# Kernel optimization log

Measured on AMD Instinct MI355X. Metric: run time of the kernel, lower is better.

Reference implementation:

```python
import jax, jax.numpy as jnp
import numpy as np

N = 200000
C = 128
VOX = 0.05
EPS = 1e-5
OFFSETS = np.array([[dz, dy, dx] for dz in (-1, 0, 1) for dy in (-1, 0, 1) for dx in (-1, 0, 1)], dtype=np.int64)


def setup_inputs() -> dict:
    key = jax.random.key(0)
    ks = jax.random.split(key, 8)
    gp = jax.random.normal(ks[0], (N, 14), jnp.float32)
    # ---- voxelization tables (int constants, computed once in numpy) ----
    pts = np.asarray(gp[:, :3], dtype=np.float64)
    vc = np.floor(pts / VOX).astype(np.int64)
    vc = vc - vc.min(axis=0)
    mx = vc.max(axis=0) + 1
    h = vc[:, 0] * mx[1] * mx[2] + vc[:, 1] * mx[2] + vc[:, 2]
    uh, inv = np.unique(h, return_inverse=True)
    M = int(uh.shape[0])
    vcoord = np.zeros((M, 3), np.int64)
    vcoord[inv] = vc  # coords identical for same hash
    nbr_idx = np.zeros((M, 27), np.int32)
    nbr_mask = np.zeros((M, 27), np.float32)
    for o in range(27):
        nc = vcoord + OFFSETS[o]
        inb = (nc >= 0).all(1) & (nc < mx).all(1)
        nh = nc[:, 0] * mx[1] * mx[2] + nc[:, 1] * mx[2] + nc[:, 2]
        pos = np.clip(np.searchsorted(uh, nh), 0, M - 1)
        found = inb & (uh[pos] == nh)
        nbr_idx[:, o] = np.where(found, pos, 0)
        nbr_mask[:, o] = found.astype(np.float32)
    s = 0.05
    return {
        'gaussian_params': gp,
        'w_enc': jax.random.normal(ks[1], (14, C), jnp.float32) * s,
        'b_enc': jnp.zeros((C,), jnp.float32),
        'ln_g': jnp.ones((C,), jnp.float32),
        'ln_b': jnp.zeros((C,), jnp.float32),
        'conv_w': jax.random.normal(ks[2], (4, 27, C, C), jnp.float32) * s,
        'bn_g': jnp.ones((4, C), jnp.float32),
        'bn_b': jnp.zeros((4, C), jnp.float32),
        'w1': jax.random.normal(ks[3], (C, C // 2), jnp.float32) * s,
        'b1': jnp.zeros((C // 2,), jnp.float32),
        'w2': jax.random.normal(ks[4], (C // 2, 14), jnp.float32) * s,
        'b2': jnp.zeros((14,), jnp.float32),
        'nbr_mask': jnp.asarray(nbr_mask),
        'inv_idx': jnp.asarray(inv.astype(np.int32)),
        'nbr_idx': jnp.asarray(nbr_idx),
        'num_voxels': M,
    }


def _bn(x, g, b):
    m = x.mean(0)
    v = x.var(0)
    return (x - m) * jax.lax.rsqrt(v + EPS) * g + b


def _subm(x, W, nbr_idx, nbr_mask):
    # submanifold 3x3x3 conv: sum over 27 offsets of masked neighbor gather @ W[o]
    out = jnp.zeros_like(x)
    for o in range(27):
        out = out + (x[nbr_idx[:, o]] * nbr_mask[:, o:o + 1]) @ W[o]
    return out


def _forward(gp, w_enc, b_enc, ln_g, ln_b, conv_w, bn_g, bn_b, w1, b1, w2, b2, nbr_mask, inv_idx, nbr_idx, num_voxels):
    # input encoder: Linear -> LayerNorm -> ReLU
    f = gp @ w_enc + b_enc
    mu = f.mean(-1, keepdims=True)
    var = f.var(-1, keepdims=True)
    f = jax.nn.relu((f - mu) * jax.lax.rsqrt(var + EPS) * ln_g + ln_b)
    # points -> voxels: segment mean (the op the torch code did with a Python loop)
    cnt = jax.ops.segment_sum(jnp.ones((gp.shape[0],), f.dtype), inv_idx, num_segments=num_voxels)
    x = jax.ops.segment_sum(f, inv_idx, num_segments=num_voxels) / cnt[:, None]
    # 2 residual sparse conv blocks (BN uses batch stats, training-mode forward)
    for blk in range(2):
        idn = x
        out = _subm(x, conv_w[2 * blk], nbr_idx, nbr_mask)
        out = jax.nn.relu(_bn(out, bn_g[2 * blk], bn_b[2 * blk]))
        out = _subm(out, conv_w[2 * blk + 1], nbr_idx, nbr_mask)
        x = jax.nn.relu(_bn(out, bn_g[2 * blk + 1], bn_b[2 * blk + 1]) + idn)
    # voxels -> points, output head, residual add
    pf = x[inv_idx]
    delta = jax.nn.relu(pf @ w1 + b1) @ w2 + b2
    return gp[:, :14] + delta


def reference(gaussian_params, w_enc, b_enc, ln_g, ln_b, conv_w, bn_g, bn_b, w1, b1, w2, b2, nbr_mask, inv_idx, nbr_idx, num_voxels):
    return _forward(gaussian_params, w_enc, b_enc, ln_g, ln_b, conv_w, bn_g, bn_b, w1, b1, w2, b2, nbr_mask, inv_idx, nbr_idx, num_voxels)
```

## Files before the change

### kernel.cpp

```cpp
#include <hip/hip_runtime.h>

typedef __bf16 bf16x8 __attribute__((ext_vector_type(8)));
typedef float f32x16 __attribute__((ext_vector_type(16)));

#define LN_EPS 1e-5f
#define AS1 __attribute__((address_space(1)))
#define AS3 __attribute__((address_space(3)))

__device__ __forceinline__ unsigned f2bf_rne(float f) {
    unsigned x = __float_as_uint(f);
    return (x + 0x7fffu + ((x >> 16) & 1u)) >> 16;
}

__device__ __forceinline__ float bf2f(unsigned short u) {
    return __uint_as_float((unsigned)u << 16);
}

__global__ void pack_w_kernel(const float* __restrict__ cw, unsigned short* __restrict__ Wp, int E) {
    int idx = blockIdx.x * 256 + threadIdx.x;
    if (idx >= E) return;
    float v = cw[idx];
    int n  = idx & 127;
    int c  = (idx >> 7) & 127;
    int oc = idx >> 14;
    Wp[oc * 16384 + (c >> 3) * 1024 + n * 8 + (c & 7)] = (unsigned short)f2bf_rne(v);
}

__global__ void pack_w1_kernel(const float* __restrict__ w1, unsigned short* __restrict__ Wp1) {
    int idx = blockIdx.x * 256 + threadIdx.x;
    if (idx >= 8192) return;
    int k = idx >> 6, n = idx & 63;
    Wp1[(k >> 3) * 512 + n * 8 + (k & 7)] = (unsigned short)f2bf_rne(w1[k * 64 + n]);
}

__global__ void prep_nbr_kernel(const int* __restrict__ nbr_idx, const float* __restrict__ nbr_mask,
                                int* __restrict__ T, unsigned* __restrict__ act, int M) {
    int m = blockIdx.x * 256 + threadIdx.x;
    if (m >= M) return;
    unsigned bits = 0;
#pragma unroll
    for (int o = 0; o < 27; ++o) {
        bool f = nbr_mask[m * 27 + o] != 0.f;
        int g = f ? nbr_idx[m * 27 + o] : M;
        T[o * M + m] = g;
        bits |= (f ? 1u : 0u) << o;
    }
    atomicOr(&act[m >> 8], bits);
}

__global__ __launch_bounds__(256) void encode_kernel(
    const float* __restrict__ gp, const float* __restrict__ w_enc,
    const float* __restrict__ b_enc, const float* __restrict__ ln_g,
    const float* __restrict__ ln_b, const int* __restrict__ inv_idx,
    float* __restrict__ vsum, float* __restrict__ cnt, int N)
{
    int p = blockIdx.x * 4 + (threadIdx.x >> 6);
    int lane = threadIdx.x & 63;
    if (p >= N) return;
    float gv[14];
#pragma unroll
    for (int i = 0; i < 14; ++i) gv[i] = gp[p * 14 + i];
    float f0 = b_enc[lane], f1 = b_enc[lane + 64];
#pragma unroll
    for (int i = 0; i < 14; ++i) {
        f0 = fmaf(gv[i], w_enc[i * 128 + lane], f0);
        f1 = fmaf(gv[i], w_enc[i * 128 + lane + 64], f1);
    }
    float s = f0 + f1;
#pragma unroll
    for (int off = 32; off; off >>= 1) s += __shfl_xor(s, off);
    float mean = s * 0.0078125f;
    float d0 = f0 - mean, d1 = f1 - mean;
    float v = d0 * d0 + d1 * d1;
#pragma unroll
    for (int off = 32; off; off >>= 1) v += __shfl_xor(v, off);
    float rs = rsqrtf(v * 0.0078125f + LN_EPS);
    float h0 = d0 * rs * ln_g[lane] + ln_b[lane];
    float h1 = d1 * rs * ln_g[lane + 64] + ln_b[lane + 64];
    h0 = h0 > 0.f ? h0 : 0.f;
    h1 = h1 > 0.f ? h1 : 0.f;
    int vx = inv_idx[p];
    atomicAdd(&vsum[vx * 128 + lane], h0);
    atomicAdd(&vsum[vx * 128 + lane + 64], h1);
    if (lane == 0) atomicAdd(&cnt[vx], 1.0f);
}

__global__ void vox_mean_kernel(const float* __restrict__ vsum, const float* __restrict__ cnt,
                                unsigned short* __restrict__ out, int total4) {
    int idx = blockIdx.x * 256 + threadIdx.x;
    if (idx >= total4) return;
    int e0 = idx * 4;
    float r = 1.f / cnt[e0 >> 7];
    float4 v = *(const float4*)(vsum + e0);
    uint2 pk;
    pk.x = f2bf_rne(v.x * r) | (f2bf_rne(v.y * r) << 16);
    pk.y = f2bf_rne(v.z * r) | (f2bf_rne(v.w * r) << 16);
    *(uint2*)(out + e0) = pk;
}

#define STAGE_W(OFF, BUFSEL)                                                          \
    {                                                                                 \
        const uint4* WpO4 = (const uint4*)Wp + (OFF) * 2048;                          \
        _Pragma("unroll")                                                             \
        for (int rep = 0; rep < 8; ++rep) {                                           \
            __builtin_amdgcn_global_load_lds(                                         \
                (const AS1 unsigned int*)(WpO4 + rep * 256 + tid),                    \
                (AS3 unsigned int*)(Ws + (BUFSEL) * 2048 + rep * 256 + w * 64),       \
                16, 0, 0);                                                            \
        }                                                                             \
    }

#define GATHER_A(AF, G)                                                               \
    _Pragma("unroll")                                                                 \
    for (int j = 0; j < 8; ++j) (AF)[j] = xin4[(G) * 16 + 2 * j + q];

__global__ __launch_bounds__(256, 2) void subm_conv_kernel(
    const unsigned short* __restrict__ xin,
    const unsigned short* __restrict__ Wp,
    const int* __restrict__ T, const unsigned* __restrict__ act,
    float* __restrict__ yout, float* __restrict__ stats, int M)
{
    __shared__ uint4 Ws[4096];

    const int tid = threadIdx.x;
    const int lane = tid & 63;
    const int w = tid >> 6;

    const int nwg = gridDim.x;
    const int orig = blockIdx.x;
    const int xcd = orig & 7;
    const int q8 = nwg >> 3, r8 = nwg & 7;
    const int tile = (xcd < r8 ? xcd * (q8 + 1) : r8 * (q8 + 1) + (xcd - r8) * q8) + (orig >> 3);

    const int m0 = tile * 256;
    const int rw = w * 64;
    const int q = lane >> 5;
    const int l31 = lane & 31;
    int row0 = m0 + rw + l31;
    int row1 = row0 + 32;
    if (row0 >= M) row0 = M - 1;
    if (row1 >= M) row1 = M - 1;

    f32x16 acc0[4], acc1[4];
#pragma unroll
    for (int t = 0; t < 4; ++t)
#pragma unroll
        for (int r = 0; r < 16; ++r) { acc0[t][r] = 0.f; acc1[t][r] = 0.f; }

    const uint4* xin4 = (const uint4*)xin;
    unsigned amask = act[tile];

    if (amask) {
        int o = __ffs(amask) - 1; amask &= amask - 1;
        STAGE_W(o, 0);
        int g0 = T[o * M + row0];
        int g1 = T[o * M + row1];
        int buf = 0;

        while (true) {
            int onext = -1;
            if (amask) { onext = __ffs(amask) - 1; amask &= amask - 1; }

            __syncthreads();

            if (onext >= 0) STAGE_W(onext, buf ^ 1);

            uint4 af0[8], af1[8];
            GATHER_A(af0, g0);
            GATHER_A(af1, g1);

            int gn0 = 0, gn1 = 0;
            if (onext >= 0) { gn0 = T[onext * M + row0]; gn1 = T[onext * M + row1]; }

            const bf16x8* WsB = (const bf16x8*)(Ws + buf * 2048);
            __builtin_amdgcn_s_setprio(1);
#pragma unroll
            for (int ks = 0; ks < 8; ++ks) {
                int kb = (ks << 1) | q;
                bf16x8 a0 = *(const bf16x8*)&af0[ks];
                bf16x8 a1 = *(const bf16x8*)&af1[ks];
#pragma unroll
                for (int tn = 0; tn < 4; ++tn) {
                    bf16x8 b = WsB[kb * 128 + tn * 32 + l31];
                    acc0[tn] = __builtin_amdgcn_mfma_f32_32x32x16_bf16(a0, b, acc0[tn], 0, 0, 0);
                    acc1[tn] = __builtin_amdgcn_mfma_f32_32x32x16_bf16(a1, b, acc1[tn], 0, 0, 0);
                }
            }
            __builtin_amdgcn_s_setprio(0);

            if (onext < 0) break;
            o = onext; g0 = gn0; g1 = gn1; buf ^= 1;
        }
    }

#pragma unroll
    for (int tn = 0; tn < 4; ++tn) {
        int col = tn * 32 + l31;
        float s = 0.f, sq = 0.f;
#pragma unroll
        for (int r = 0; r < 16; ++r) {
            int rloc = (r & 3) + 8 * (r >> 2) + 4 * q + rw;
            int grow = m0 + rloc;
            float v = (grow < M) ? acc0[tn][r] : 0.f;
            if (grow < M) yout[grow * 128 + col] = v;
            s += v; sq += v * v;
        }
#pragma unroll
        for (int r = 0; r < 16; ++r) {
            int rloc = (r & 3) + 8 * (r >> 2) + 4 * q + rw + 32;
            int grow = m0 + rloc;
            float v = (grow < M) ? acc1[tn][r] : 0.f;
            if (grow < M) yout[grow * 128 + col] = v;
            s += v; sq += v * v;
        }
        s += __shfl_xor(s, 32);
        sq += __shfl_xor(sq, 32);
        if (lane < 32) {
            atomicAdd(&stats[col], s);
            atomicAdd(&stats[128 + col], sq);
        }
    }
}

__global__ void bn_relu_kernel(const float* __restrict__ y, const float* __restrict__ stats,
                               const float* __restrict__ g, const float* __restrict__ b,
                               unsigned short* __restrict__ out, int total4, float invM) {
    int idx = blockIdx.x * 256 + threadIdx.x;
    if (idx >= total4) return;
    int e0 = idx * 4;
    int c0 = e0 & 127;
    float4 yv = *(const float4*)(y + e0);
    float h[4];
    const float* yp = (const float*)&yv;
#pragma unroll
    for (int j = 0; j < 4; ++j) {
        int c = c0 + j;
        float mean = stats[c] * invM;
        float var = stats[128 + c] * invM - mean * mean;
        float sc = g[c] * rsqrtf(var + LN_EPS);
        float sh = b[c] - mean * sc;
        float vv = yp[j] * sc + sh;
        h[j] = vv > 0.f ? vv : 0.f;
    }
    uint2 pk;
    pk.x = f2bf_rne(h[0]) | (f2bf_rne(h[1]) << 16);
    pk.y = f2bf_rne(h[2]) | (f2bf_rne(h[3]) << 16);
    *(uint2*)(out + e0) = pk;
}

__global__ void bn_relu_res_kernel(const float* __restrict__ y, const float* __restrict__ stats,
                                   const float* __restrict__ g, const float* __restrict__ b,
                                   const unsigned short* __restrict__ idn,
                                   unsigned short* __restrict__ out, int total4, float invM) {
    int idx = blockIdx.x * 256 + threadIdx.x;
    if (idx >= total4) return;
    int e0 = idx * 4;
    int c0 = e0 & 127;
    float4 yv = *(const float4*)(y + e0);
    uint2 iv = *(const uint2*)(idn + e0);
    float id[4];
    id[0] = __uint_as_float(iv.x << 16);
    id[1] = __uint_as_float(iv.x & 0xffff0000u);
    id[2] = __uint_as_float(iv.y << 16);
    id[3] = __uint_as_float(iv.y & 0xffff0000u);
    float h[4];
    const float* yp = (const float*)&yv;
#pragma unroll
    for (int j = 0; j < 4; ++j) {
        int c = c0 + j;
        float mean = stats[c] * invM;
        float var = stats[128 + c] * invM - mean * mean;
        float sc = g[c] * rsqrtf(var + LN_EPS);
        float sh = b[c] - mean * sc;
        float vv = yp[j] * sc + sh + id[j];
        h[j] = vv > 0.f ? vv : 0.f;
    }
    uint2 pk;
    pk.x = f2bf_rne(h[0]) | (f2bf_rne(h[1]) << 16);
    pk.y = f2bf_rne(h[2]) | (f2bf_rne(h[3]) << 16);
    *(uint2*)(out + e0) = pk;
}

__global__ __launch_bounds__(256) void head_vox_kernel(
    const unsigned short* __restrict__ A,
    const unsigned short* __restrict__ Wp1,
    const float* __restrict__ b1, const float* __restrict__ w2,
    const float* __restrict__ b2, float* __restrict__ Dv, int M)
{
    __shared__ uint4 W1s[1024];
    __shared__ unsigned short Hs[8192];
    __shared__ float w2s[896];

    const int tid = threadIdx.x;
    const int lane = tid & 63;
    const int w = tid >> 6;
    const int m0 = blockIdx.x * 128;
    const int rw = w * 32;
    const int q = lane >> 5;
    const int l31 = lane & 31;
    int myrow = m0 + rw + l31;
    if (myrow > M) myrow = M;

#pragma unroll
    for (int rep = 0; rep < 4; ++rep) {
        __builtin_amdgcn_global_load_lds(
            (const AS1 unsigned int*)((const uint4*)Wp1 + rep * 256 + tid),
            (AS3 unsigned int*)(W1s + rep * 256 + w * 64), 16, 0, 0);
    }
    for (int i = tid; i < 896; i += 256) w2s[i] = w2[i];

    const uint4* xin4 = (const uint4*)A;
    uint4 af[8];
#pragma unroll
    for (int j = 0; j < 8; ++j) af[j] = xin4[myrow * 16 + 2 * j + q];

    f32x16 acc[2];
#pragma unroll
    for (int t = 0; t < 2; ++t)
#pragma unroll
        for (int r = 0; r < 16; ++r) acc[t][r] = 0.f;

    __syncthreads();

#pragma unroll
    for (int ks = 0; ks < 8; ++ks) {
        int kb = (ks << 1) | q;
        bf16x8 a = *(const bf16x8*)&af[ks];
#pragma unroll
        for (int tn = 0; tn < 2; ++tn) {
            bf16x8 b = ((const bf16x8*)W1s)[kb * 64 + tn * 32 + l31];
            acc[tn] = __builtin_amdgcn_mfma_f32_32x32x16_bf16(a, b, acc[tn], 0, 0, 0);
        }
    }

#pragma unroll
    for (int tn = 0; tn < 2; ++tn) {
        int col = tn * 32 + l31;
        float bias = b1[col];
        int ch = col >> 3, ce = col & 7;
#pragma unroll
        for (int r = 0; r < 16; ++r) {
            int rloc = (r & 3) + 8 * (r >> 2) + 4 * q + rw;
            float v = acc[tn][r] + bias;
            v = v > 0.f ? v : 0.f;
            Hs[rloc * 64 + (ch ^ (rloc & 7)) * 8 + ce] = (unsigned short)f2bf_rne(v);
        }
    }
    __syncthreads();

    int r2 = tid >> 1;
    int c0 = (tid & 1) * 7;
    float o[7];
#pragma unroll
    for (int j = 0; j < 7; ++j) o[j] = b2[c0 + j];
#pragma unroll
    for (int c = 0; c < 8; ++c) {
        bf16x8 hv = ((const bf16x8*)Hs)[r2 * 8 + (c ^ (r2 & 7))];
#pragma unroll
        for (int e = 0; e < 8; ++e) {
            float h = bf2f(((const unsigned short*)&hv)[e]);
            int k = c * 8 + e;
#pragma unroll
            for (int j = 0; j < 7; ++j) o[j] = fmaf(h, w2s[k * 14 + c0 + j], o[j]);
        }
    }
    int grow = m0 + r2;
    if (grow < M) {
#pragma unroll
        for (int j = 0; j < 7; ++j) Dv[grow * 14 + c0 + j] = o[j];
    }
}

__global__ void head_scatter_kernel(const float* __restrict__ gp, const float* __restrict__ Dv,
                                    const int* __restrict__ inv_idx, float* __restrict__ out, int N) {
    int p = blockIdx.x * 256 + threadIdx.x;
    if (p >= N) return;
    int vx = inv_idx[p];
#pragma unroll
    for (int c = 0; c < 14; ++c) out[p * 14 + c] = gp[p * 14 + c] + Dv[vx * 14 + c];
}

extern "C" void kernel_launch(void* const* d_in, const int* in_sizes, int n_in,
                              void* d_out, int out_size, void* d_ws, size_t ws_size,
                              hipStream_t stream) {
    const float* gp       = (const float*)d_in[0];
    const float* w_enc    = (const float*)d_in[1];
    const float* b_enc    = (const float*)d_in[2];
    const float* ln_g     = (const float*)d_in[3];
    const float* ln_b     = (const float*)d_in[4];
    const float* conv_w   = (const float*)d_in[5];
    const float* bn_g     = (const float*)d_in[6];
    const float* bn_b     = (const float*)d_in[7];
    const float* w1       = (const float*)d_in[8];
    const float* b1       = (const float*)d_in[9];
    const float* w2       = (const float*)d_in[10];
    const float* b2       = (const float*)d_in[11];
    const float* nbr_mask = (const float*)d_in[12];
    const int*   inv_idx  = (const int*)d_in[13];
    const int*   nbr_idx  = (const int*)d_in[14];

    const int N = in_sizes[0] / 14;
    const int M = in_sizes[12] / 27;
    const int ntiles = (M + 127) / 128;
    const int ntiles256 = (M + 255) / 256;

    char* ws = (char*)d_ws;
    size_t off = 0;
    unsigned short* Wp = (unsigned short*)(ws + off); off += (size_t)4 * 27 * 16384 * 2;
    unsigned short* A  = (unsigned short*)(ws + off); off += (size_t)(M + 1) * 128 * 2;
    unsigned short* H  = (unsigned short*)(ws + off); off += (size_t)(M + 1) * 128 * 2;
    float* Yraw  = (float*)(ws + off);
    size_t zoff = off;
    off += (size_t)M * 128 * 4;
    float* cnt   = (float*)(ws + off); off += (size_t)M * 4;
    float* stats = (float*)(ws + off); off += 4 * 256 * 4;
    unsigned* act = (unsigned*)(ws + off); off += (size_t)ntiles * 4;
    size_t zbytes = off - zoff;
    int* T = (int*)(ws + off); off += (size_t)27 * M * 4;
    unsigned short* Wp1 = (unsigned short*)(ws + off); off += 8192 * 2;
    float* Dv = Yraw;

    hipMemsetAsync(Yraw, 0, zbytes, stream);
    hipMemsetAsync(A + (size_t)M * 128, 0, 256, stream);
    hipMemsetAsync(H + (size_t)M * 128, 0, 256, stream);

    const int E = 4 * 27 * 128 * 128;
    pack_w_kernel<<<(E + 255) / 256, 256, 0, stream>>>(conv_w, Wp, E);
    pack_w1_kernel<<<32, 256, 0, stream>>>(w1, Wp1);
    prep_nbr_kernel<<<(M + 255) / 256, 256, 0, stream>>>(nbr_idx, nbr_mask, T, act, M);
    encode_kernel<<<(N + 3) / 4, 256, 0, stream>>>(gp, w_enc, b_enc, ln_g, ln_b, inv_idx, Yraw, cnt, N);
    const int total4 = M * 32;
    vox_mean_kernel<<<(total4 + 255) / 256, 256, 0, stream>>>(Yraw, cnt, A, total4);

    const float invM = 1.f / (float)M;
    for (int blk = 0; blk < 2; ++blk) {
        int c0 = 2 * blk, c1 = 2 * blk + 1;
        subm_conv_kernel<<<ntiles256, 256, 0, stream>>>(
            A, Wp + (size_t)c0 * 27 * 16384, T, act, Yraw, stats + c0 * 256, M);
        bn_relu_kernel<<<(total4 + 255) / 256, 256, 0, stream>>>(
            Yraw, stats + c0 * 256, bn_g + c0 * 128, bn_b + c0 * 128, H, total4, invM);
        subm_conv_kernel<<<ntiles256, 256, 0, stream>>>(
            H, Wp + (size_t)c1 * 27 * 16384, T, act, Yraw, stats + c1 * 256, M);
        bn_relu_res_kernel<<<(total4 + 255) / 256, 256, 0, stream>>>(
            Yraw, stats + c1 * 256, bn_g + c1 * 128, bn_b + c1 * 128, A, A, total4, invM);
    }
    head_vox_kernel<<<ntiles, 256, 0, stream>>>(A, Wp1, b1, w2, b2, Dv, M);
    head_scatter_kernel<<<(N + 255) / 256, 256, 0, stream>>>(gp, Dv, inv_idx, (float*)d_out, N);
}
```

Measured before the change: 1.480 ms.

## Load conv weights directly from global with per-wave offset masks and register prefetch

The sparse conv kernel no longer stages each offset's weight slice into LDS with block-wide barriers. Each wave now reads its B fragments straight from global memory (relying on L2 and cache) and prefetches the next k-step's weights and the next offset's gathered activations into registers. Active-offset masks are built per 64-row wave instead of per 256-row tile, so each wave can skip offsets independently without barriers. The trade-offs are heavier global and cache traffic for weights, higher register pressure with the launch-bounds occupancy hint removed, and a plain copy loop replacing the async LDS load in the head kernel.

Measured after the change: 1.424 ms. 1.04x faster.

```diff
diff --git a/kernel.cpp b/kernel.cpp
--- a/kernel.cpp
+++ b/kernel.cpp
@@ -4,8 +4,6 @@
 typedef float f32x16 __attribute__((ext_vector_type(16)));
 
 #define LN_EPS 1e-5f
-#define AS1 __attribute__((address_space(1)))
-#define AS3 __attribute__((address_space(3)))
 
 __device__ __forceinline__ unsigned f2bf_rne(float f) {
     unsigned x = __float_as_uint(f);
@@ -34,7 +32,7 @@
 }
 
 __global__ void prep_nbr_kernel(const int* __restrict__ nbr_idx, const float* __restrict__ nbr_mask,
-                                int* __restrict__ T, unsigned* __restrict__ act, int M) {
+                                int* __restrict__ T, unsigned* __restrict__ act64, int M) {
     int m = blockIdx.x * 256 + threadIdx.x;
     if (m >= M) return;
     unsigned bits = 0;
@@ -45,7 +43,7 @@
         T[o * M + m] = g;
         bits |= (f ? 1u : 0u) << o;
     }
-    atomicOr(&act[m >> 8], bits);
+    atomicOr(&act64[m >> 6], bits);
 }
 
 __global__ __launch_bounds__(256) void encode_kernel(
@@ -98,30 +96,12 @@
     *(uint2*)(out + e0) = pk;
 }
 
-#define STAGE_W(OFF, BUFSEL)                                                          \
-    {                                                                                 \
-        const uint4* WpO4 = (const uint4*)Wp + (OFF) * 2048;                          \
-        _Pragma("unroll")                                                             \
-        for (int rep = 0; rep < 8; ++rep) {                                           \
-            __builtin_amdgcn_global_load_lds(                                         \
-                (const AS1 unsigned int*)(WpO4 + rep * 256 + tid),                    \
-                (AS3 unsigned int*)(Ws + (BUFSEL) * 2048 + rep * 256 + w * 64),       \
-                16, 0, 0);                                                            \
-        }                                                                             \
-    }
-
-#define GATHER_A(AF, G)                                                               \
-    _Pragma("unroll")                                                                 \
-    for (int j = 0; j < 8; ++j) (AF)[j] = xin4[(G) * 16 + 2 * j + q];
-
-__global__ __launch_bounds__(256, 2) void subm_conv_kernel(
+__global__ __launch_bounds__(256) void subm_conv_kernel(
     const unsigned short* __restrict__ xin,
     const unsigned short* __restrict__ Wp,
-    const int* __restrict__ T, const unsigned* __restrict__ act,
+    const int* __restrict__ T, const unsigned* __restrict__ act64,
     float* __restrict__ yout, float* __restrict__ stats, int M)
 {
-    __shared__ uint4 Ws[4096];
-
     const int tid = threadIdx.x;
     const int lane = tid & 63;
     const int w = tid >> 6;
@@ -148,48 +128,69 @@
         for (int r = 0; r < 16; ++r) { acc0[t][r] = 0.f; acc1[t][r] = 0.f; }
 
     const uint4* xin4 = (const uint4*)xin;
-    unsigned amask = act[tile];
+    const bf16x8* WpB = (const bf16x8*)Wp;
+
+    unsigned amask = act64[tile * 4 + w];
 
     if (amask) {
         int o = __ffs(amask) - 1; amask &= amask - 1;
-        STAGE_W(o, 0);
-        int g0 = T[o * M + row0];
-        int g1 = T[o * M + row1];
-        int buf = 0;
+        int h0 = T[o * M + row0], h1 = T[o * M + row1];
+        uint4 af0[8], af1[8];
+#pragma unroll
+        for (int j = 0; j < 8; ++j) {
+            af0[j] = xin4[h0 * 16 + 2 * j + q];
+            af1[j] = xin4[h1 * 16 + 2 * j + q];
+        }
+        int o1 = -1;
+        if (amask) {
+            o1 = __ffs(amask) - 1; amask &= amask - 1;
+            h0 = T[o1 * M + row0]; h1 = T[o1 * M + row1];
+        }
 
         while (true) {
-            int onext = -1;
-            if (amask) { onext = __ffs(amask) - 1; amask &= amask - 1; }
-
-            __syncthreads();
-
-            if (onext >= 0) STAGE_W(onext, buf ^ 1);
-
-            uint4 af0[8], af1[8];
-            GATHER_A(af0, g0);
-            GATHER_A(af1, g1);
-
-            int gn0 = 0, gn1 = 0;
-            if (onext >= 0) { gn0 = T[onext * M + row0]; gn1 = T[onext * M + row1]; }
-
-            const bf16x8* WsB = (const bf16x8*)(Ws + buf * 2048);
+            int o2 = -1, i0 = 0, i1 = 0;
+            if (amask) {
+                o2 = __ffs(amask) - 1; amask &= amask - 1;
+                i0 = T[o2 * M + row0]; i1 = T[o2 * M + row1];
+            }
+
+            const bf16x8* Bo = WpB + (size_t)o * 2048;
+            const bool more = (o1 >= 0);
+
             __builtin_amdgcn_s_setprio(1);
+            bf16x8 bn0 = Bo[q * 128 + l31];
+            bf16x8 bn1 = Bo[q * 128 + 32 + l31];
+            bf16x8 bn2 = Bo[q * 128 + 64 + l31];
+            bf16x8 bn3 = Bo[q * 128 + 96 + l31];
 #pragma unroll
             for (int ks = 0; ks < 8; ++ks) {
-                int kb = (ks << 1) | q;
+                bf16x8 bc0 = bn0, bc1 = bn1, bc2 = bn2, bc3 = bn3;
+                if (ks < 7) {
+                    int kbn = ((ks + 1) << 1) | q;
+                    bn0 = Bo[kbn * 128 + l31];
+                    bn1 = Bo[kbn * 128 + 32 + l31];
+                    bn2 = Bo[kbn * 128 + 64 + l31];
+                    bn3 = Bo[kbn * 128 + 96 + l31];
+                }
                 bf16x8 a0 = *(const bf16x8*)&af0[ks];
                 bf16x8 a1 = *(const bf16x8*)&af1[ks];
-#pragma unroll
-                for (int tn = 0; tn < 4; ++tn) {
-                    bf16x8 b = WsB[kb * 128 + tn * 32 + l31];
-                    acc0[tn] = __builtin_amdgcn_mfma_f32_32x32x16_bf16(a0, b, acc0[tn], 0, 0, 0);
-                    acc1[tn] = __builtin_amdgcn_mfma_f32_32x32x16_bf16(a1, b, acc1[tn], 0, 0, 0);
+                if (more) {
+                    af0[ks] = xin4[h0 * 16 + 2 * ks + q];
+                    af1[ks] = xin4[h1 * 16 + 2 * ks + q];
                 }
+                acc0[0] = __builtin_amdgcn_mfma_f32_32x32x16_bf16(a0, bc0, acc0[0], 0, 0, 0);
+                acc1[0] = __builtin_amdgcn_mfma_f32_32x32x16_bf16(a1, bc0, acc1[0], 0, 0, 0);
+                acc0[1] = __builtin_amdgcn_mfma_f32_32x32x16_bf16(a0, bc1, acc0[1], 0, 0, 0);
+                acc1[1] = __builtin_amdgcn_mfma_f32_32x32x16_bf16(a1, bc1, acc1[1], 0, 0, 0);
+                acc0[2] = __builtin_amdgcn_mfma_f32_32x32x16_bf16(a0, bc2, acc0[2], 0, 0, 0);
+                acc1[2] = __builtin_amdgcn_mfma_f32_32x32x16_bf16(a1, bc2, acc1[2], 0, 0, 0);
+                acc0[3] = __builtin_amdgcn_mfma_f32_32x32x16_bf16(a0, bc3, acc0[3], 0, 0, 0);
+                acc1[3] = __builtin_amdgcn_mfma_f32_32x32x16_bf16(a1, bc3, acc1[3], 0, 0, 0);
             }
             __builtin_amdgcn_s_setprio(0);
 
-            if (onext < 0) break;
-            o = onext; g0 = gn0; g1 = gn1; buf ^= 1;
+            if (!more) break;
+            o = o1; o1 = o2; h0 = i0; h1 = i1;
         }
     }
 
@@ -301,12 +302,7 @@
     int myrow = m0 + rw + l31;
     if (myrow > M) myrow = M;
 
-#pragma unroll
-    for (int rep = 0; rep < 4; ++rep) {
-        __builtin_amdgcn_global_load_lds(
-            (const AS1 unsigned int*)((const uint4*)Wp1 + rep * 256 + tid),
-            (AS3 unsigned int*)(W1s + rep * 256 + w * 64), 16, 0, 0);
-    }
+    for (int i = tid; i < 1024; i += 256) W1s[i] = ((const uint4*)Wp1)[i];
     for (int i = tid; i < 896; i += 256) w2s[i] = w2[i];
 
     const uint4* xin4 = (const uint4*)A;
@@ -414,7 +410,7 @@
     off += (size_t)M * 128 * 4;
     float* cnt   = (float*)(ws + off); off += (size_t)M * 4;
     float* stats = (float*)(ws + off); off += 4 * 256 * 4;
-    unsigned* act = (unsigned*)(ws + off); off += (size_t)ntiles * 4;
+    unsigned* act64 = (unsigned*)(ws + off); off += (size_t)ntiles256 * 4 * 4;
     size_t zbytes = off - zoff;
     int* T = (int*)(ws + off); off += (size_t)27 * M * 4;
     unsigned short* Wp1 = (unsigned short*)(ws + off); off += 8192 * 2;
@@ -427,7 +423,7 @@
     const int E = 4 * 27 * 128 * 128;
     pack_w_kernel<<<(E + 255) / 256, 256, 0, stream>>>(conv_w, Wp, E);
     pack_w1_kernel<<<32, 256, 0, stream>>>(w1, Wp1);
-    prep_nbr_kernel<<<(M + 255) / 256, 256, 0, stream>>>(nbr_idx, nbr_mask, T, act, M);
+    prep_nbr_kernel<<<(M + 255) / 256, 256, 0, stream>>>(nbr_idx, nbr_mask, T, act64, M);
     encode_kernel<<<(N + 3) / 4, 256, 0, stream>>>(gp, w_enc, b_enc, ln_g, ln_b, inv_idx, Yraw, cnt, N);
     const int total4 = M * 32;
     vox_mean_kernel<<<(total4 + 255) / 256, 256, 0, stream>>>(Yraw, cnt, A, total4);
@@ -436,11 +432,11 @@
     for (int blk = 0; blk < 2; ++blk) {
         int c0 = 2 * blk, c1 = 2 * blk + 1;
         subm_conv_kernel<<<ntiles256, 256, 0, stream>>>(
-            A, Wp + (size_t)c0 * 27 * 16384, T, act, Yraw, stats + c0 * 256, M);
+            A, Wp + (size_t)c0 * 27 * 16384, T, act64, Yraw, stats + c0 * 256, M);
         bn_relu_kernel<<<(total4 + 255) / 256, 256, 0, stream>>>(
             Yraw, stats + c0 * 256, bn_g + c0 * 128, bn_b + c0 * 128, H, total4, invM);
         subm_conv_kernel<<<ntiles256, 256, 0, stream>>>(
-            H, Wp + (size_t)c1 * 27 * 16384, T, act, Yraw, stats + c1 * 256, M);
+            H, Wp + (size_t)c1 * 27 * 16384, T, act64, Yraw, stats + c1 * 256, M);
         bn_relu_res_kernel<<<(total4 + 255) / 256, 256, 0, stream>>>(
             Yraw, stats + c1 * 256, bn_g + c1 * 128, bn_b + c1 * 128, A, A, total4, invM);
     }
```
